# Kernel optimization log

Hardware: AMD Instinct MI355X
Metric: run time of the kernel (lower is better)

Reference implementation:

```python
import jax, jax.numpy as jnp
import numpy as np

N = 100000
E = 1600000
IN_C, HID_C, OUT_C = 128, 128, 64


def setup_inputs() -> dict:
    key = jax.random.key(0)
    ks = jax.random.split(key, 8)
    x = jax.random.normal(ks[0], (N, IN_C), dtype=jnp.float32)
    edge_index = jax.random.randint(ks[1], (2, E), 0, N, dtype=jnp.int64)
    s = 1.0 / np.sqrt(IN_C)
    s2 = 1.0 / np.sqrt(HID_C)
    return {
        "x": x,
        "edge_index": edge_index,
        # layer 1: SAGEConv(in=128, out=128): lin_l (neighbor, with bias), lin_r (root, no bias)
        "W_l1": jax.random.uniform(ks[2], (IN_C, HID_C), jnp.float32, -s, s),
        "b_l1": jnp.zeros((HID_C,), jnp.float32),
        "W_r1": jax.random.uniform(ks[3], (IN_C, HID_C), jnp.float32, -s, s),
        # layer 2: SAGEConv(in=128, out=64)
        "W_l2": jax.random.uniform(ks[4], (HID_C, OUT_C), jnp.float32, -s2, s2),
        "b_l2": jnp.zeros((OUT_C,), jnp.float32),
        "W_r2": jax.random.uniform(ks[5], (HID_C, OUT_C), jnp.float32, -s2, s2),
    }


def _sage_conv(x, src, dst, W_l, b_l, W_r, n_nodes):
    # mean aggregation of source-node features at target nodes
    msg = x[src]                                    # [E, d] gather
    agg = jax.ops.segment_sum(msg, dst, num_segments=n_nodes)          # [N, d]
    cnt = jax.ops.segment_sum(jnp.ones((src.shape[0], 1), x.dtype), dst,
                              num_segments=n_nodes)                    # [N, 1]
    mean = agg / jnp.maximum(cnt, 1.0)
    # out = lin_l(mean_neighbors) + lin_r(x_self)
    return mean @ W_l + b_l + x @ W_r


def reference(x, edge_index, W_l1, b_l1, W_r1, W_l2, b_l2, W_r2):
    src, dst = edge_index[0], edge_index[1]
    n = x.shape[0]
    h = _sage_conv(x, src, dst, W_l1, b_l1, W_r1, n)
    h = jax.nn.relu(h)  # dropout is identity in eval mode
    out = _sage_conv(h, src, dst, W_l2, b_l2, W_r2, n)
    return out
```

## Files before the change

kernel.cpp:

```cpp
#include <hip/hip_runtime.h>
#include <hip/hip_bf16.h>
#include <stdint.h>

#define IN_C 128
#define HID_C 128
#define OUT_C 64

#define NBUCK 256
#define BSH 9
#define EPB 2048

typedef _Float16 h8 __attribute__((ext_vector_type(8)));
typedef _Float16 h2 __attribute__((ext_vector_type(2)));
typedef float f4 __attribute__((ext_vector_type(4)));
typedef float f2 __attribute__((ext_vector_type(2)));
typedef unsigned u4 __attribute__((ext_vector_type(4)));

__device__ inline float h2lo(unsigned v){ h2 t = __builtin_bit_cast(h2, v); return (float)t[0]; }
__device__ inline float h2hi(unsigned v){ h2 t = __builtin_bit_cast(h2, v); return (float)t[1]; }
__device__ inline unsigned packh2(float a, float b){ h2 t; t[0]=(_Float16)a; t[1]=(_Float16)b; return __builtin_bit_cast(unsigned, t); }

__device__ inline void pack_one(const float* __restrict__ W, int C, _Float16* __restrict__ outp, int tid){
    int l = tid & 63;
    int f = tid >> 6;
    int NJT = C / 16;
    int kt = f / NJT;
    int jt = f - kt*NJT;
    int kbase = kt*32 + (l >> 4)*8;
    int col   = jt*16 + (l & 15);
    h8 o;
    #pragma unroll
    for (int r = 0; r < 8; ++r) o[r] = (_Float16)W[(kbase + r)*C + col];
    ((h8*)outp)[f*64 + l] = o;
}

__global__ __launch_bounds__(256) void k_front(const int* __restrict__ dst, int E, int NBLK,
                                               int* __restrict__ histT,
                                               const float* __restrict__ x,
                                               uint2* __restrict__ x8, int n8,
                                               const float* __restrict__ Wl1, const float* __restrict__ Wr1,
                                               const float* __restrict__ Wl2, const float* __restrict__ Wr2,
                                               _Float16* __restrict__ wl1p, _Float16* __restrict__ wr1p,
                                               _Float16* __restrict__ wl2p, _Float16* __restrict__ wr2p){
    __shared__ int h[NBUCK];
    int bid = blockIdx.x, t = threadIdx.x;
    if (bid < NBLK){
        h[t] = 0; __syncthreads();
        int e0 = bid*EPB, e1 = min(E, e0 + EPB);
        for (int e = e0 + t; e < e1; e += 256) atomicAdd(&h[((unsigned)dst[e]) >> BSH], 1);
        __syncthreads();
        histT[t*NBLK + bid] = h[t];
    } else if (bid < NBLK + 24){
        int tid = (bid - NBLK)*256 + t;
        if (tid < 2048)        pack_one(Wl1, 128, wl1p, tid);
        else if (tid < 4096)   pack_one(Wr1, 128, wr1p, tid - 2048);
        else if (tid < 5120)   pack_one(Wl2,  64, wl2p, tid - 4096);
        else if (tid < 6144)   pack_one(Wr2,  64, wr2p, tid - 5120);
    } else {
        int g = (bid - NBLK - 24)*256 + t;
        if (g < n8){
            const f4* xp = (const f4*)(x + (size_t)g*8);
            f4 a = xp[0], b = xp[1];
            int w0 = __builtin_amdgcn_cvt_pk_fp8_f32(a[0], a[1], 0, false);
            w0     = __builtin_amdgcn_cvt_pk_fp8_f32(a[2], a[3], w0, true);
            int w1 = __builtin_amdgcn_cvt_pk_fp8_f32(b[0], b[1], 0, false);
            w1     = __builtin_amdgcn_cvt_pk_fp8_f32(b[2], b[3], w1, true);
            uint2 p; p.x = (unsigned)w0; p.y = (unsigned)w1;
            x8[g] = p;
        }
    }
}

__global__ void k_scanA(const int* __restrict__ cnt, int* __restrict__ tmp, int* __restrict__ bsum, int n){
    __shared__ int s[256];
    int t = threadIdx.x, g = blockIdx.x*256 + t;
    int v = (g < n) ? cnt[g] : 0;
    s[t] = v; __syncthreads();
    for (int off = 1; off < 256; off <<= 1){
        int a = (t >= off) ? s[t-off] : 0;
        __syncthreads();
        s[t] += a;
        __syncthreads();
    }
    int excl = (t == 0) ? 0 : s[t-1];
    if (g < n) tmp[g] = excl;
    if (t == 255) bsum[blockIdx.x] = s[255];
}

__global__ void k_scanB(int* __restrict__ bsum, int nb){
    __shared__ int s[1024];
    int t = threadIdx.x;
    int v = (t < nb) ? bsum[t] : 0;
    s[t] = v; __syncthreads();
    for (int off = 1; off < 1024; off <<= 1){
        int a = (t >= off) ? s[t-off] : 0;
        __syncthreads();
        s[t] += a;
        __syncthreads();
    }
    int excl = (t == 0) ? 0 : s[t-1];
    if (t < nb) bsum[t] = excl;
}

__global__ __launch_bounds__(256) void k_scatter(const int* __restrict__ src, const int* __restrict__ dst,
                                                 int E, const int* __restrict__ tmp, const int* __restrict__ bsum,
                                                 int NBLK, unsigned* __restrict__ sorted){
    __shared__ int off[NBUCK];
    int t = threadIdx.x;
    int g = t*NBLK + blockIdx.x;
    off[t] = tmp[g] + bsum[g >> 8];
    __syncthreads();
    int e0 = blockIdx.x*EPB, e1 = min(E, e0 + EPB);
    for (int e = e0 + t; e < e1; e += 256){
        int d = dst[e];
        int b = ((unsigned)d) >> BSH;
        int p = atomicAdd(&off[b], 1);
        sorted[p] = (unsigned)src[e] | (((unsigned)(d & ((1<<BSH)-1))) << 17);
    }
}

__global__ __launch_bounds__(512) void k_csr(const unsigned* __restrict__ sorted,
                                             const int* __restrict__ tmp, const int* __restrict__ bsum,
                                             int NBLK, int E, int N,
                                             int* __restrict__ csr, int* __restrict__ row_start){
    __shared__ int cnt[512];
    __shared__ int sc[512];
    int b = blockIdx.x, t = threadIdx.x;
    int i0 = b*NBLK;
    int bs = tmp[i0] + bsum[i0 >> 8];
    int be = (b == NBUCK-1) ? E : (tmp[i0 + NBLK] + bsum[(i0 + NBLK) >> 8]);
    cnt[t] = 0; __syncthreads();
    for (int e = bs + t; e < be; e += 512) atomicAdd(&cnt[sorted[e] >> 17], 1);
    __syncthreads();
    sc[t] = cnt[t]; __syncthreads();
    for (int off = 1; off < 512; off <<= 1){
        int a = (t >= off) ? sc[t-off] : 0;
        __syncthreads();
        sc[t] += a;
        __syncthreads();
    }
    int excl = sc[t] - cnt[t];
    int nid = (b << BSH) + t;
    if (nid < N) row_start[nid] = bs + excl;
    if (t == 0 && b == (N >> BSH)) row_start[N] = E;
    __syncthreads();
    cnt[t] = excl;
    __syncthreads();
    for (int e = bs + t; e < be; e += 512){
        unsigned v = sorted[e];
        int dl = v >> 17;
        int p = atomicAdd(&cnt[dl], 1);
        csr[bs + p] = (int)(v & 0x1FFFFu);
    }
}

__global__ void k_agg1(const int* __restrict__ row_start, const int* __restrict__ csr,
                       const uint2* __restrict__ x8, unsigned* __restrict__ mh32, int n){
    int node = (int)((blockIdx.x*(unsigned)blockDim.x + threadIdx.x) >> 4);
    int c = threadIdx.x & 15;
    if (node >= n) return;
    int base = row_start[node], end = row_start[node+1];
    int deg = end - base;
    f2 a0={0.f,0.f}, a1={0.f,0.f}, a2={0.f,0.f}, a3={0.f,0.f};
    f2 b0={0.f,0.f}, b1={0.f,0.f}, b2={0.f,0.f}, b3={0.f,0.f};
    int i = base;
    for (; i + 7 < end; i += 8){
        int e0 = csr[i],   e1 = csr[i+1], e2 = csr[i+2], e3 = csr[i+3];
        int e4 = csr[i+4], e5 = csr[i+5], e6 = csr[i+6], e7 = csr[i+7];
        uint2 v0 = x8[(size_t)e0*16 + c];
        uint2 v1 = x8[(size_t)e1*16 + c];
        uint2 v2 = x8[(size_t)e2*16 + c];
        uint2 v3 = x8[(size_t)e3*16 + c];
        uint2 v4 = x8[(size_t)e4*16 + c];
        uint2 v5 = x8[(size_t)e5*16 + c];
        uint2 v6 = x8[(size_t)e6*16 + c];
        uint2 v7 = x8[(size_t)e7*16 + c];
        a0 += __builtin_amdgcn_cvt_pk_f32_fp8(v0.x, false);
        a1 += __builtin_amdgcn_cvt_pk_f32_fp8(v0.x, true);
        a2 += __builtin_amdgcn_cvt_pk_f32_fp8(v0.y, false);
        a3 += __builtin_amdgcn_cvt_pk_f32_fp8(v0.y, true);
        b0 += __builtin_amdgcn_cvt_pk_f32_fp8(v1.x, false);
        b1 += __builtin_amdgcn_cvt_pk_f32_fp8(v1.x, true);
        b2 += __builtin_amdgcn_cvt_pk_f32_fp8(v1.y, false);
        b3 += __builtin_amdgcn_cvt_pk_f32_fp8(v1.y, true);
        a0 += __builtin_amdgcn_cvt_pk_f32_fp8(v2.x, false);
        a1 += __builtin_amdgcn_cvt_pk_f32_fp8(v2.x, true);
        a2 += __builtin_amdgcn_cvt_pk_f32_fp8(v2.y, false);
        a3 += __builtin_amdgcn_cvt_pk_f32_fp8(v2.y, true);
        b0 += __builtin_amdgcn_cvt_pk_f32_fp8(v3.x, false);
        b1 += __builtin_amdgcn_cvt_pk_f32_fp8(v3.x, true);
        b2 += __builtin_amdgcn_cvt_pk_f32_fp8(v3.y, false);
        b3 += __builtin_amdgcn_cvt_pk_f32_fp8(v3.y, true);
        a0 += __builtin_amdgcn_cvt_pk_f32_fp8(v4.x, false);
        a1 += __builtin_amdgcn_cvt_pk_f32_fp8(v4.x, true);
        a2 += __builtin_amdgcn_cvt_pk_f32_fp8(v4.y, false);
        a3 += __builtin_amdgcn_cvt_pk_f32_fp8(v4.y, true);
        b0 += __builtin_amdgcn_cvt_pk_f32_fp8(v5.x, false);
        b1 += __builtin_amdgcn_cvt_pk_f32_fp8(v5.x, true);
        b2 += __builtin_amdgcn_cvt_pk_f32_fp8(v5.y, false);
        b3 += __builtin_amdgcn_cvt_pk_f32_fp8(v5.y, true);
        a0 += __builtin_amdgcn_cvt_pk_f32_fp8(v6.x, false);
        a1 += __builtin_amdgcn_cvt_pk_f32_fp8(v6.x, true);
        a2 += __builtin_amdgcn_cvt_pk_f32_fp8(v6.y, false);
        a3 += __builtin_amdgcn_cvt_pk_f32_fp8(v6.y, true);
        b0 += __builtin_amdgcn_cvt_pk_f32_fp8(v7.x, false);
        b1 += __builtin_amdgcn_cvt_pk_f32_fp8(v7.x, true);
        b2 += __builtin_amdgcn_cvt_pk_f32_fp8(v7.y, false);
        b3 += __builtin_amdgcn_cvt_pk_f32_fp8(v7.y, true);
    }
    for (; i + 3 < end; i += 4){
        int e0 = csr[i], e1 = csr[i+1], e2 = csr[i+2], e3 = csr[i+3];
        uint2 v0 = x8[(size_t)e0*16 + c];
        uint2 v1 = x8[(size_t)e1*16 + c];
        uint2 v2 = x8[(size_t)e2*16 + c];
        uint2 v3 = x8[(size_t)e3*16 + c];
        a0 += __builtin_amdgcn_cvt_pk_f32_fp8(v0.x, false);
        a1 += __builtin_amdgcn_cvt_pk_f32_fp8(v0.x, true);
        a2 += __builtin_amdgcn_cvt_pk_f32_fp8(v0.y, false);
        a3 += __builtin_amdgcn_cvt_pk_f32_fp8(v0.y, true);
        b0 += __builtin_amdgcn_cvt_pk_f32_fp8(v1.x, false);
        b1 += __builtin_amdgcn_cvt_pk_f32_fp8(v1.x, true);
        b2 += __builtin_amdgcn_cvt_pk_f32_fp8(v1.y, false);
        b3 += __builtin_amdgcn_cvt_pk_f32_fp8(v1.y, true);
        a0 += __builtin_amdgcn_cvt_pk_f32_fp8(v2.x, false);
        a1 += __builtin_amdgcn_cvt_pk_f32_fp8(v2.x, true);
        a2 += __builtin_amdgcn_cvt_pk_f32_fp8(v2.y, false);
        a3 += __builtin_amdgcn_cvt_pk_f32_fp8(v2.y, true);
        b0 += __builtin_amdgcn_cvt_pk_f32_fp8(v3.x, false);
        b1 += __builtin_amdgcn_cvt_pk_f32_fp8(v3.x, true);
        b2 += __builtin_amdgcn_cvt_pk_f32_fp8(v3.y, false);
        b3 += __builtin_amdgcn_cvt_pk_f32_fp8(v3.y, true);
    }
    for (; i < end; ++i){
        int e = csr[i];
        uint2 v = x8[(size_t)e*16 + c];
        a0 += __builtin_amdgcn_cvt_pk_f32_fp8(v.x, false);
        a1 += __builtin_amdgcn_cvt_pk_f32_fp8(v.x, true);
        a2 += __builtin_amdgcn_cvt_pk_f32_fp8(v.y, false);
        a3 += __builtin_amdgcn_cvt_pk_f32_fp8(v.y, true);
    }
    a0 += b0; a1 += b1; a2 += b2; a3 += b3;
    float sc = 1.0f / (float)max(deg, 1);
    u4 o;
    o[0] = packh2(a0[0]*sc, a0[1]*sc);
    o[1] = packh2(a1[0]*sc, a1[1]*sc);
    o[2] = packh2(a2[0]*sc, a2[1]*sc);
    o[3] = packh2(a3[0]*sc, a3[1]*sc);
    *(u4*)(mh32 + (size_t)node*64 + 4*c) = o;
}

__global__ __launch_bounds__(512, 4) void k_gemm_fused(
    const _Float16* __restrict__ A0,
    const float* __restrict__ X,
    const h8* __restrict__ B0,
    const h8* __restrict__ B1,
    const float* __restrict__ bias1,
    const h8* __restrict__ W2l,
    const h8* __restrict__ W2r,
    const float* __restrict__ bias2,
    unsigned* __restrict__ P8,
    uint2* __restrict__ Qh,
    int M)
{
    __shared__ h8 shB[4096];
    int tid = threadIdx.x;
    #pragma unroll
    for (int i = 0; i < 4; ++i) shB[i*512 + tid] = B0[i*512 + tid];
    #pragma unroll
    for (int i = 0; i < 4; ++i) shB[2048 + i*512 + tid] = B1[i*512 + tid];
    __syncthreads();

    int wid = tid >> 6, lane = tid & 63;
    int m0 = (blockIdx.x*8 + wid) * 16;
    if (m0 >= M) return;
    int m = lane & 15, kg = lane >> 4;
    int rowc = min(m0 + m, M-1);

    f4 acc[8];
    #pragma unroll
    for (int j = 0; j < 8; ++j) acc[j] = (f4)0.0f;

    #pragma unroll
    for (int kt = 0; kt < 4; ++kt){
        h8 nf = *(const h8*)(A0 + (size_t)rowc*128 + kt*32 + kg*8);
        #pragma unroll
        for (int j = 0; j < 8; ++j){
            h8 wf = shB[(kt*8 + j)*64 + lane];
            acc[j] = __builtin_amdgcn_mfma_f32_16x16x32_f16(wf, nf, acc[j], 0, 0, 0);
        }
    }
    #pragma unroll
    for (int kt = 0; kt < 4; ++kt){
        const float* xr = X + (size_t)rowc*128 + kt*32 + kg*8;
        f4 xa = *(const f4*)(xr);
        f4 xb = *(const f4*)(xr + 4);
        h8 nf;
        nf[0]=(_Float16)xa[0]; nf[1]=(_Float16)xa[1]; nf[2]=(_Float16)xa[2]; nf[3]=(_Float16)xa[3];
        nf[4]=(_Float16)xb[0]; nf[5]=(_Float16)xb[1]; nf[6]=(_Float16)xb[2]; nf[7]=(_Float16)xb[3];
        #pragma unroll
        for (int j = 0; j < 8; ++j){
            h8 wf = shB[2048 + (kt*8 + j)*64 + lane];
            acc[j] = __builtin_amdgcn_mfma_f32_16x16x32_f16(wf, nf, acc[j], 0, 0, 0);
        }
    }

    unsigned hreg[16];
    #pragma unroll
    for (int j = 0; j < 8; ++j){
        f4 bb = *(const f4*)(bias1 + j*16 + kg*4);
        float v0 = acc[j][0] + bb[0]; v0 = v0 > 0.f ? v0 : 0.f;
        float v1 = acc[j][1] + bb[1]; v1 = v1 > 0.f ? v1 : 0.f;
        float v2 = acc[j][2] + bb[2]; v2 = v2 > 0.f ? v2 : 0.f;
        float v3 = acc[j][3] + bb[3]; v3 = v3 > 0.f ? v3 : 0.f;
        hreg[2*j]   = packh2(v0, v1);
        hreg[2*j+1] = packh2(v2, v3);
    }

    f4 accP[4], accQ[4];
    #pragma unroll
    for (int j = 0; j < 4; ++j){ accP[j] = (f4)0.0f; accQ[j] = (f4)0.0f; }

    int srcA = ((kg & 1) * 2) * 16 + m;
    int srcB = srcA + 16;
    bool hi = (kg >> 1) & 1;

    #pragma unroll
    for (int kt = 0; kt < 4; ++kt){
        unsigned sA0 = (unsigned)__shfl((int)hreg[4*kt+0], srcA, 64);
        unsigned sA1 = (unsigned)__shfl((int)hreg[4*kt+1], srcA, 64);
        unsigned sA2 = (unsigned)__shfl((int)hreg[4*kt+2], srcA, 64);
        unsigned sA3 = (unsigned)__shfl((int)hreg[4*kt+3], srcA, 64);
        unsigned sB0 = (unsigned)__shfl((int)hreg[4*kt+0], srcB, 64);
        unsigned sB1 = (unsigned)__shfl((int)hreg[4*kt+1], srcB, 64);
        unsigned sB2 = (unsigned)__shfl((int)hreg[4*kt+2], srcB, 64);
        unsigned sB3 = (unsigned)__shfl((int)hreg[4*kt+3], srcB, 64);
        u4 u;
        u[0] = hi ? sA2 : sA0;
        u[1] = hi ? sA3 : sA1;
        u[2] = hi ? sB2 : sB0;
        u[3] = hi ? sB3 : sB1;
        h8 hf = __builtin_bit_cast(h8, u);
        #pragma unroll
        for (int j2 = 0; j2 < 4; ++j2){
            accP[j2] = __builtin_amdgcn_mfma_f32_16x16x32_f16(W2l[(kt*4 + j2)*64 + lane], hf, accP[j2], 0, 0, 0);
            accQ[j2] = __builtin_amdgcn_mfma_f32_16x16x32_f16(W2r[(kt*4 + j2)*64 + lane], hf, accQ[j2], 0, 0, 0);
        }
    }

    int node = m0 + m;
    if (node < M){
        #pragma unroll
        for (int j2 = 0; j2 < 4; ++j2){
            int f = j2*16 + kg*4;
            int p8 = __builtin_amdgcn_cvt_pk_fp8_f32(accP[j2][0], accP[j2][1], 0, false);
            p8     = __builtin_amdgcn_cvt_pk_fp8_f32(accP[j2][2], accP[j2][3], p8, true);
            P8[(size_t)node*16 + j2*4 + kg] = (unsigned)p8;
            f4 bb2 = *(const f4*)(bias2 + f);
            uint2 qp;
            qp.x = packh2(accQ[j2][0] + bb2[0], accQ[j2][1] + bb2[1]);
            qp.y = packh2(accQ[j2][2] + bb2[2], accQ[j2][3] + bb2[3]);
            Qh[(size_t)node*16 + j2*4 + kg] = qp;
        }
    }
}

__global__ void k_agg2f(const int* __restrict__ row_start, const int* __restrict__ csr,
                        const unsigned* __restrict__ p8, const uint2* __restrict__ Qh,
                        float* __restrict__ out, int n){
    int node = (int)((blockIdx.x*(unsigned)blockDim.x + threadIdx.x) >> 4);
    int c = threadIdx.x & 15;
    if (node >= n) return;
    int base = row_start[node], end = row_start[node+1];
    int deg = end - base;
    f2 a0={0.f,0.f}, a1={0.f,0.f}, b0={0.f,0.f}, b1={0.f,0.f};
    f2 c0={0.f,0.f}, c1={0.f,0.f}, d0={0.f,0.f}, d1={0.f,0.f};
    int i = base;
    for (; i + 7 < end; i += 8){
        int e0 = csr[i],   e1 = csr[i+1], e2 = csr[i+2], e3 = csr[i+3];
        int e4 = csr[i+4], e5 = csr[i+5], e6 = csr[i+6], e7 = csr[i+7];
        unsigned v0 = p8[(size_t)e0*16 + c];
        unsigned v1 = p8[(size_t)e1*16 + c];
        unsigned v2 = p8[(size_t)e2*16 + c];
        unsigned v3 = p8[(size_t)e3*16 + c];
        unsigned v4 = p8[(size_t)e4*16 + c];
        unsigned v5 = p8[(size_t)e5*16 + c];
        unsigned v6 = p8[(size_t)e6*16 + c];
        unsigned v7 = p8[(size_t)e7*16 + c];
        a0 += __builtin_amdgcn_cvt_pk_f32_fp8(v0, false);
        a1 += __builtin_amdgcn_cvt_pk_f32_fp8(v0, true);
        b0 += __builtin_amdgcn_cvt_pk_f32_fp8(v1, false);
        b1 += __builtin_amdgcn_cvt_pk_f32_fp8(v1, true);
        c0 += __builtin_amdgcn_cvt_pk_f32_fp8(v2, false);
        c1 += __builtin_amdgcn_cvt_pk_f32_fp8(v2, true);
        d0 += __builtin_amdgcn_cvt_pk_f32_fp8(v3, false);
        d1 += __builtin_amdgcn_cvt_pk_f32_fp8(v3, true);
        a0 += __builtin_amdgcn_cvt_pk_f32_fp8(v4, false);
        a1 += __builtin_amdgcn_cvt_pk_f32_fp8(v4, true);
        b0 += __builtin_amdgcn_cvt_pk_f32_fp8(v5, false);
        b1 += __builtin_amdgcn_cvt_pk_f32_fp8(v5, true);
        c0 += __builtin_amdgcn_cvt_pk_f32_fp8(v6, false);
        c1 += __builtin_amdgcn_cvt_pk_f32_fp8(v6, true);
        d0 += __builtin_amdgcn_cvt_pk_f32_fp8(v7, false);
        d1 += __builtin_amdgcn_cvt_pk_f32_fp8(v7, true);
    }
    for (; i + 3 < end; i += 4){
        int e0 = csr[i], e1 = csr[i+1], e2 = csr[i+2], e3 = csr[i+3];
        unsigned v0 = p8[(size_t)e0*16 + c];
        unsigned v1 = p8[(size_t)e1*16 + c];
        unsigned v2 = p8[(size_t)e2*16 + c];
        unsigned v3 = p8[(size_t)e3*16 + c];
        a0 += __builtin_amdgcn_cvt_pk_f32_fp8(v0, false);
        a1 += __builtin_amdgcn_cvt_pk_f32_fp8(v0, true);
        b0 += __builtin_amdgcn_cvt_pk_f32_fp8(v1, false);
        b1 += __builtin_amdgcn_cvt_pk_f32_fp8(v1, true);
        c0 += __builtin_amdgcn_cvt_pk_f32_fp8(v2, false);
        c1 += __builtin_amdgcn_cvt_pk_f32_fp8(v2, true);
        d0 += __builtin_amdgcn_cvt_pk_f32_fp8(v3, false);
        d1 += __builtin_amdgcn_cvt_pk_f32_fp8(v3, true);
    }
    for (; i < end; ++i){
        int e = csr[i];
        unsigned v = p8[(size_t)e*16 + c];
        a0 += __builtin_amdgcn_cvt_pk_f32_fp8(v, false);
        a1 += __builtin_amdgcn_cvt_pk_f32_fp8(v, true);
    }
    a0 += b0 + c0 + d0;
    a1 += b1 + c1 + d1;
    float sc = 1.0f / (float)max(deg, 1);
    uint2 qh = Qh[(size_t)node*16 + c];
    f4 o;
    o[0] = a0[0]*sc + h2lo(qh.x);
    o[1] = a0[1]*sc + h2hi(qh.x);
    o[2] = a1[0]*sc + h2lo(qh.y);
    o[3] = a1[1]*sc + h2hi(qh.y);
    *(f4*)(out + (size_t)node*64 + 4*c) = o;
}

extern "C" void kernel_launch(void* const* d_in, const int* in_sizes, int n_in,
                              void* d_out, int out_size, void* d_ws, size_t ws_size,
                              hipStream_t stream) {
    const float* x   = (const float*)d_in[0];
    const int*   ei  = (const int*)d_in[1];
    const float* Wl1 = (const float*)d_in[2];
    const float* bl1 = (const float*)d_in[3];
    const float* Wr1 = (const float*)d_in[4];
    const float* Wl2 = (const float*)d_in[5];
    const float* bl2 = (const float*)d_in[6];
    const float* Wr2 = (const float*)d_in[7];

    const int N = in_sizes[0] / IN_C;
    const int E = in_sizes[1] / 2;
    const int* src = ei;
    const int* dst = ei + E;

    const int NBLK = (E + EPB - 1) / EPB;
    const int n_s  = NBUCK * NBLK;

    char* w = (char*)d_ws;
    size_t off = 0;
    auto alloc = [&](size_t bytes) -> char* {
        char* p = w + off;
        off = (off + bytes + 255) & ~(size_t)255;
        return p;
    };
    int* histT      = (int*)alloc((size_t)n_s*4);
    int* tmp        = (int*)alloc((size_t)n_s*4);
    int* bsum       = (int*)alloc(4096);
    unsigned* sorted= (unsigned*)alloc((size_t)E*4);
    int* csr        = (int*)alloc((size_t)E*4);
    int* row_start  = (int*)alloc((size_t)(N+1)*4);
    unsigned* x8    = (unsigned*)alloc((size_t)N*IN_C);
    _Float16* m1h   = (_Float16*)alloc((size_t)N*IN_C*2);
    unsigned* p8    = (unsigned*)alloc((size_t)N*OUT_C);
    unsigned* qh    = (unsigned*)alloc((size_t)N*OUT_C*2);
    _Float16* wl1p  = (_Float16*)alloc(4*8*64*8*2);
    _Float16* wr1p  = (_Float16*)alloc(4*8*64*8*2);
    _Float16* wl2p  = (_Float16*)alloc(4*4*64*8*2);
    _Float16* wr2p  = (_Float16*)alloc(4*4*64*8*2);

    const int SB = (n_s + 255) / 256;
    const int n8 = N*IN_C/8;
    const int CVB = (n8 + 255)/256;

    k_front  <<<NBLK + 24 + CVB, 256, 0, stream>>>(dst, E, NBLK, histT,
                                                   x, (uint2*)x8, n8,
                                                   Wl1, Wr1, Wl2, Wr2, wl1p, wr1p, wl2p, wr2p);
    k_scanA  <<<SB, 256, 0, stream>>>(histT, tmp, bsum, n_s);
    k_scanB  <<<1, 1024, 0, stream>>>(bsum, SB);
    k_scatter<<<NBLK, 256, 0, stream>>>(src, dst, E, tmp, bsum, NBLK, sorted);
    k_csr    <<<NBUCK, 512, 0, stream>>>(sorted, tmp, bsum, NBLK, E, N, csr, row_start);

    const int AB = (N + 15) / 16;
    k_agg1<<<AB, 256, 0, stream>>>(row_start, csr, (const uint2*)x8, (unsigned*)m1h, N);

    const int GB2 = (N + 127)/128;
    k_gemm_fused<<<GB2, 512, 0, stream>>>(m1h, x, (const h8*)wl1p, (const h8*)wr1p, bl1,
                                          (const h8*)wl2p, (const h8*)wr2p, bl2,
                                          p8, (uint2*)qh, N);

    k_agg2f<<<AB, 256, 0, stream>>>(row_start, csr, p8, (const uint2*)qh, (float*)d_out, N);
}
```

Measured before the change: 148.1 us.

## Fuse layer-1 neighbor aggregation into the fused GEMM kernel via shared memory

Removes the separate k_agg1 kernel and computes the mean-aggregated fp16 neighbor features for each wave's 16 rows directly inside k_gemm_fused. The results go into a per-wave shared-memory tile with an XOR swizzle, and the MFMA A operand is read from there. This avoids writing and re-reading the N x 128 fp16 intermediate in global memory and saves one kernel launch. In exchange, shared memory per block grows by 32 KB, launch bounds drop to 2 blocks per CU, and the latency-bound gather now runs inside the GEMM kernel at lower occupancy.

```diff
diff --git a/kernel.cpp b/kernel.cpp
--- a/kernel.cpp
+++ b/kernel.cpp
@@ -154,103 +154,9 @@
     }
 }
 
-__global__ void k_agg1(const int* __restrict__ row_start, const int* __restrict__ csr,
-                       const uint2* __restrict__ x8, unsigned* __restrict__ mh32, int n){
-    int node = (int)((blockIdx.x*(unsigned)blockDim.x + threadIdx.x) >> 4);
-    int c = threadIdx.x & 15;
-    if (node >= n) return;
-    int base = row_start[node], end = row_start[node+1];
-    int deg = end - base;
-    f2 a0={0.f,0.f}, a1={0.f,0.f}, a2={0.f,0.f}, a3={0.f,0.f};
-    f2 b0={0.f,0.f}, b1={0.f,0.f}, b2={0.f,0.f}, b3={0.f,0.f};
-    int i = base;
-    for (; i + 7 < end; i += 8){
-        int e0 = csr[i],   e1 = csr[i+1], e2 = csr[i+2], e3 = csr[i+3];
-        int e4 = csr[i+4], e5 = csr[i+5], e6 = csr[i+6], e7 = csr[i+7];
-        uint2 v0 = x8[(size_t)e0*16 + c];
-        uint2 v1 = x8[(size_t)e1*16 + c];
-        uint2 v2 = x8[(size_t)e2*16 + c];
-        uint2 v3 = x8[(size_t)e3*16 + c];
-        uint2 v4 = x8[(size_t)e4*16 + c];
-        uint2 v5 = x8[(size_t)e5*16 + c];
-        uint2 v6 = x8[(size_t)e6*16 + c];
-        uint2 v7 = x8[(size_t)e7*16 + c];
-        a0 += __builtin_amdgcn_cvt_pk_f32_fp8(v0.x, false);
-        a1 += __builtin_amdgcn_cvt_pk_f32_fp8(v0.x, true);
-        a2 += __builtin_amdgcn_cvt_pk_f32_fp8(v0.y, false);
-        a3 += __builtin_amdgcn_cvt_pk_f32_fp8(v0.y, true);
-        b0 += __builtin_amdgcn_cvt_pk_f32_fp8(v1.x, false);
-        b1 += __builtin_amdgcn_cvt_pk_f32_fp8(v1.x, true);
-        b2 += __builtin_amdgcn_cvt_pk_f32_fp8(v1.y, false);
-        b3 += __builtin_amdgcn_cvt_pk_f32_fp8(v1.y, true);
-        a0 += __builtin_amdgcn_cvt_pk_f32_fp8(v2.x, false);
-        a1 += __builtin_amdgcn_cvt_pk_f32_fp8(v2.x, true);
-        a2 += __builtin_amdgcn_cvt_pk_f32_fp8(v2.y, false);
-        a3 += __builtin_amdgcn_cvt_pk_f32_fp8(v2.y, true);
-        b0 += __builtin_amdgcn_cvt_pk_f32_fp8(v3.x, false);
-        b1 += __builtin_amdgcn_cvt_pk_f32_fp8(v3.x, true);
-        b2 += __builtin_amdgcn_cvt_pk_f32_fp8(v3.y, false);
-        b3 += __builtin_amdgcn_cvt_pk_f32_fp8(v3.y, true);
-        a0 += __builtin_amdgcn_cvt_pk_f32_fp8(v4.x, false);
-        a1 += __builtin_amdgcn_cvt_pk_f32_fp8(v4.x, true);
-        a2 += __builtin_amdgcn_cvt_pk_f32_fp8(v4.y, false);
-        a3 += __builtin_amdgcn_cvt_pk_f32_fp8(v4.y, true);
-        b0 += __builtin_amdgcn_cvt_pk_f32_fp8(v5.x, false);
-        b1 += __builtin_amdgcn_cvt_pk_f32_fp8(v5.x, true);
-        b2 += __builtin_amdgcn_cvt_pk_f32_fp8(v5.y, false);
-        b3 += __builtin_amdgcn_cvt_pk_f32_fp8(v5.y, true);
-        a0 += __builtin_amdgcn_cvt_pk_f32_fp8(v6.x, false);
-        a1 += __builtin_amdgcn_cvt_pk_f32_fp8(v6.x, true);
-        a2 += __builtin_amdgcn_cvt_pk_f32_fp8(v6.y, false);
-        a3 += __builtin_amdgcn_cvt_pk_f32_fp8(v6.y, true);
-        b0 += __builtin_amdgcn_cvt_pk_f32_fp8(v7.x, false);
-        b1 += __builtin_amdgcn_cvt_pk_f32_fp8(v7.x, true);
-        b2 += __builtin_amdgcn_cvt_pk_f32_fp8(v7.y, false);
-        b3 += __builtin_amdgcn_cvt_pk_f32_fp8(v7.y, true);
-    }
-    for (; i + 3 < end; i += 4){
-        int e0 = csr[i], e1 = csr[i+1], e2 = csr[i+2], e3 = csr[i+3];
-        uint2 v0 = x8[(size_t)e0*16 + c];
-        uint2 v1 = x8[(size_t)e1*16 + c];
-        uint2 v2 = x8[(size_t)e2*16 + c];
-        uint2 v3 = x8[(size_t)e3*16 + c];
-        a0 += __builtin_amdgcn_cvt_pk_f32_fp8(v0.x, false);
-        a1 += __builtin_amdgcn_cvt_pk_f32_fp8(v0.x, true);
-        a2 += __builtin_amdgcn_cvt_pk_f32_fp8(v0.y, false);
-        a3 += __builtin_amdgcn_cvt_pk_f32_fp8(v0.y, true);
-        b0 += __builtin_amdgcn_cvt_pk_f32_fp8(v1.x, false);
-        b1 += __builtin_amdgcn_cvt_pk_f32_fp8(v1.x, true);
-        b2 += __builtin_amdgcn_cvt_pk_f32_fp8(v1.y, false);
-        b3 += __builtin_amdgcn_cvt_pk_f32_fp8(v1.y, true);
-        a0 += __builtin_amdgcn_cvt_pk_f32_fp8(v2.x, false);
-        a1 += __builtin_amdgcn_cvt_pk_f32_fp8(v2.x, true);
-        a2 += __builtin_amdgcn_cvt_pk_f32_fp8(v2.y, false);
-        a3 += __builtin_amdgcn_cvt_pk_f32_fp8(v2.y, true);
-        b0 += __builtin_amdgcn_cvt_pk_f32_fp8(v3.x, false);
-        b1 += __builtin_amdgcn_cvt_pk_f32_fp8(v3.x, true);
-        b2 += __builtin_amdgcn_cvt_pk_f32_fp8(v3.y, false);
-        b3 += __builtin_amdgcn_cvt_pk_f32_fp8(v3.y, true);
-    }
-    for (; i < end; ++i){
-        int e = csr[i];
-        uint2 v = x8[(size_t)e*16 + c];
-        a0 += __builtin_amdgcn_cvt_pk_f32_fp8(v.x, false);
-        a1 += __builtin_amdgcn_cvt_pk_f32_fp8(v.x, true);
-        a2 += __builtin_amdgcn_cvt_pk_f32_fp8(v.y, false);
-        a3 += __builtin_amdgcn_cvt_pk_f32_fp8(v.y, true);
-    }
-    a0 += b0; a1 += b1; a2 += b2; a3 += b3;
-    float sc = 1.0f / (float)max(deg, 1);
-    u4 o;
-    o[0] = packh2(a0[0]*sc, a0[1]*sc);
-    o[1] = packh2(a1[0]*sc, a1[1]*sc);
-    o[2] = packh2(a2[0]*sc, a2[1]*sc);
-    o[3] = packh2(a3[0]*sc, a3[1]*sc);
-    *(u4*)(mh32 + (size_t)node*64 + 4*c) = o;
-}
-
-__global__ __launch_bounds__(512, 4) void k_gemm_fused(
-    const _Float16* __restrict__ A0,
+__global__ __launch_bounds__(512, 2) void k_gemm_fused(
+    const int* __restrict__ row_start, const int* __restrict__ csr,
+    const uint2* __restrict__ x8,
     const float* __restrict__ X,
     const h8* __restrict__ B0,
     const h8* __restrict__ B1,
@@ -263,6 +169,7 @@
     int M)
 {
     __shared__ h8 shB[4096];
+    __shared__ unsigned shM[8][1024];
     int tid = threadIdx.x;
     #pragma unroll
     for (int i = 0; i < 4; ++i) shB[i*512 + tid] = B0[i*512 + tid];
@@ -276,13 +183,111 @@
     int m = lane & 15, kg = lane >> 4;
     int rowc = min(m0 + m, M-1);
 
+    unsigned* myM = &shM[wid][0];
+    {
+        int c = lane & 15;
+        #pragma unroll 1
+        for (int p = 0; p < 4; ++p){
+            int slot = p*4 + (lane >> 4);
+            int node = min(m0 + slot, M-1);
+            int base = row_start[node], end = row_start[node+1];
+            int deg = end - base;
+            f2 a0={0.f,0.f}, a1={0.f,0.f}, a2={0.f,0.f}, a3={0.f,0.f};
+            f2 b0={0.f,0.f}, b1={0.f,0.f}, b2={0.f,0.f}, b3={0.f,0.f};
+            int i = base;
+            for (; i + 7 < end; i += 8){
+                int e0 = csr[i],   e1 = csr[i+1], e2 = csr[i+2], e3 = csr[i+3];
+                int e4 = csr[i+4], e5 = csr[i+5], e6 = csr[i+6], e7 = csr[i+7];
+                uint2 v0 = x8[(size_t)e0*16 + c];
+                uint2 v1 = x8[(size_t)e1*16 + c];
+                uint2 v2 = x8[(size_t)e2*16 + c];
+                uint2 v3 = x8[(size_t)e3*16 + c];
+                uint2 v4 = x8[(size_t)e4*16 + c];
+                uint2 v5 = x8[(size_t)e5*16 + c];
+                uint2 v6 = x8[(size_t)e6*16 + c];
+                uint2 v7 = x8[(size_t)e7*16 + c];
+                a0 += __builtin_amdgcn_cvt_pk_f32_fp8(v0.x, false);
+                a1 += __builtin_amdgcn_cvt_pk_f32_fp8(v0.x, true);
+                a2 += __builtin_amdgcn_cvt_pk_f32_fp8(v0.y, false);
+                a3 += __builtin_amdgcn_cvt_pk_f32_fp8(v0.y, true);
+                b0 += __builtin_amdgcn_cvt_pk_f32_fp8(v1.x, false);
+                b1 += __builtin_amdgcn_cvt_pk_f32_fp8(v1.x, true);
+                b2 += __builtin_amdgcn_cvt_pk_f32_fp8(v1.y, false);
+                b3 += __builtin_amdgcn_cvt_pk_f32_fp8(v1.y, true);
+                a0 += __builtin_amdgcn_cvt_pk_f32_fp8(v2.x, false);
+                a1 += __builtin_amdgcn_cvt_pk_f32_fp8(v2.x, true);
+                a2 += __builtin_amdgcn_cvt_pk_f32_fp8(v2.y, false);
+                a3 += __builtin_amdgcn_cvt_pk_f32_fp8(v2.y, true);
+                b0 += __builtin_amdgcn_cvt_pk_f32_fp8(v3.x, false);
+                b1 += __builtin_amdgcn_cvt_pk_f32_fp8(v3.x, true);
+                b2 += __builtin_amdgcn_cvt_pk_f32_fp8(v3.y, false);
+                b3 += __builtin_amdgcn_cvt_pk_f32_fp8(v3.y, true);
+                a0 += __builtin_amdgcn_cvt_pk_f32_fp8(v4.x, false);
+                a1 += __builtin_amdgcn_cvt_pk_f32_fp8(v4.x, true);
+                a2 += __builtin_amdgcn_cvt_pk_f32_fp8(v4.y, false);
+                a3 += __builtin_amdgcn_cvt_pk_f32_fp8(v4.y, true);
+                b0 += __builtin_amdgcn_cvt_pk_f32_fp8(v5.x, false);
+                b1 += __builtin_amdgcn_cvt_pk_f32_fp8(v5.x, true);
+                b2 += __builtin_amdgcn_cvt_pk_f32_fp8(v5.y, false);
+                b3 += __builtin_amdgcn_cvt_pk_f32_fp8(v5.y, true);
+                a0 += __builtin_amdgcn_cvt_pk_f32_fp8(v6.x, false);
+                a1 += __builtin_amdgcn_cvt_pk_f32_fp8(v6.x, true);
+                a2 += __builtin_amdgcn_cvt_pk_f32_fp8(v6.y, false);
+                a3 += __builtin_amdgcn_cvt_pk_f32_fp8(v6.y, true);
+                b0 += __builtin_amdgcn_cvt_pk_f32_fp8(v7.x, false);
+                b1 += __builtin_amdgcn_cvt_pk_f32_fp8(v7.x, true);
+                b2 += __builtin_amdgcn_cvt_pk_f32_fp8(v7.y, false);
+                b3 += __builtin_amdgcn_cvt_pk_f32_fp8(v7.y, true);
+            }
+            for (; i + 3 < end; i += 4){
+                int e0 = csr[i], e1 = csr[i+1], e2 = csr[i+2], e3 = csr[i+3];
+                uint2 v0 = x8[(size_t)e0*16 + c];
+                uint2 v1 = x8[(size_t)e1*16 + c];
+                uint2 v2 = x8[(size_t)e2*16 + c];
+                uint2 v3 = x8[(size_t)e3*16 + c];
+                a0 += __builtin_amdgcn_cvt_pk_f32_fp8(v0.x, false);
+                a1 += __builtin_amdgcn_cvt_pk_f32_fp8(v0.x, true);
+                a2 += __builtin_amdgcn_cvt_pk_f32_fp8(v0.y, false);
+                a3 += __builtin_amdgcn_cvt_pk_f32_fp8(v0.y, true);
+                b0 += __builtin_amdgcn_cvt_pk_f32_fp8(v1.x, false);
+                b1 += __builtin_amdgcn_cvt_pk_f32_fp8(v1.x, true);
+                b2 += __builtin_amdgcn_cvt_pk_f32_fp8(v1.y, false);
+                b3 += __builtin_amdgcn_cvt_pk_f32_fp8(v1.y, true);
+                a0 += __builtin_amdgcn_cvt_pk_f32_fp8(v2.x, false);
+                a1 += __builtin_amdgcn_cvt_pk_f32_fp8(v2.x, true);
+                a2 += __builtin_amdgcn_cvt_pk_f32_fp8(v2.y, false);
+                a3 += __builtin_amdgcn_cvt_pk_f32_fp8(v2.y, true);
+                b0 += __builtin_amdgcn_cvt_pk_f32_fp8(v3.x, false);
+                b1 += __builtin_amdgcn_cvt_pk_f32_fp8(v3.x, true);
+                b2 += __builtin_amdgcn_cvt_pk_f32_fp8(v3.y, false);
+                b3 += __builtin_amdgcn_cvt_pk_f32_fp8(v3.y, true);
+            }
+            for (; i < end; ++i){
+                int e = csr[i];
+                uint2 v = x8[(size_t)e*16 + c];
+                a0 += __builtin_amdgcn_cvt_pk_f32_fp8(v.x, false);
+                a1 += __builtin_amdgcn_cvt_pk_f32_fp8(v.x, true);
+                a2 += __builtin_amdgcn_cvt_pk_f32_fp8(v.y, false);
+                a3 += __builtin_amdgcn_cvt_pk_f32_fp8(v.y, true);
+            }
+            a0 += b0; a1 += b1; a2 += b2; a3 += b3;
+            float sc = 1.0f / (float)max(deg, 1);
+            u4 o;
+            o[0] = packh2(a0[0]*sc, a0[1]*sc);
+            o[1] = packh2(a1[0]*sc, a1[1]*sc);
+            o[2] = packh2(a2[0]*sc, a2[1]*sc);
+            o[3] = packh2(a3[0]*sc, a3[1]*sc);
+            *(u4*)&myM[slot*64 + ((c*4) ^ ((slot&7)<<2))] = o;
+        }
+    }
+
     f4 acc[8];
     #pragma unroll
     for (int j = 0; j < 8; ++j) acc[j] = (f4)0.0f;
 
     #pragma unroll
     for (int kt = 0; kt < 4; ++kt){
-        h8 nf = *(const h8*)(A0 + (size_t)rowc*128 + kt*32 + kg*8);
+        h8 nf = *(const h8*)&myM[m*64 + ((kt*16 + kg*4) ^ ((m&7)<<2))];
         #pragma unroll
         for (int j = 0; j < 8; ++j){
             h8 wf = shB[(kt*8 + j)*64 + lane];
@@ -352,9 +357,9 @@
         #pragma unroll
         for (int j2 = 0; j2 < 4; ++j2){
             int f = j2*16 + kg*4;
-            int p8 = __builtin_amdgcn_cvt_pk_fp8_f32(accP[j2][0], accP[j2][1], 0, false);
-            p8     = __builtin_amdgcn_cvt_pk_fp8_f32(accP[j2][2], accP[j2][3], p8, true);
-            P8[(size_t)node*16 + j2*4 + kg] = (unsigned)p8;
+            int p8v = __builtin_amdgcn_cvt_pk_fp8_f32(accP[j2][0], accP[j2][1], 0, false);
+            p8v     = __builtin_amdgcn_cvt_pk_fp8_f32(accP[j2][2], accP[j2][3], p8v, true);
+            P8[(size_t)node*16 + j2*4 + kg] = (unsigned)p8v;
             f4 bb2 = *(const f4*)(bias2 + f);
             uint2 qp;
             qp.x = packh2(accQ[j2][0] + bb2[0], accQ[j2][1] + bb2[1]);
@@ -470,7 +475,6 @@
     int* csr        = (int*)alloc((size_t)E*4);
     int* row_start  = (int*)alloc((size_t)(N+1)*4);
     unsigned* x8    = (unsigned*)alloc((size_t)N*IN_C);
-    _Float16* m1h   = (_Float16*)alloc((size_t)N*IN_C*2);
     unsigned* p8    = (unsigned*)alloc((size_t)N*OUT_C);
     unsigned* qh    = (unsigned*)alloc((size_t)N*OUT_C*2);
     _Float16* wl1p  = (_Float16*)alloc(4*8*64*8*2);
@@ -490,13 +494,12 @@
     k_scatter<<<NBLK, 256, 0, stream>>>(src, dst, E, tmp, bsum, NBLK, sorted);
     k_csr    <<<NBUCK, 512, 0, stream>>>(sorted, tmp, bsum, NBLK, E, N, csr, row_start);
 
-    const int AB = (N + 15) / 16;
-    k_agg1<<<AB, 256, 0, stream>>>(row_start, csr, (const uint2*)x8, (unsigned*)m1h, N);
-
     const int GB2 = (N + 127)/128;
-    k_gemm_fused<<<GB2, 512, 0, stream>>>(m1h, x, (const h8*)wl1p, (const h8*)wr1p, bl1,
+    k_gemm_fused<<<GB2, 512, 0, stream>>>(row_start, csr, (const uint2*)x8, x,
+                                          (const h8*)wl1p, (const h8*)wr1p, bl1,
                                           (const h8*)wl2p, (const h8*)wr2p, bl2,
                                           p8, (uint2*)qh, N);
 
+    const int AB = (N + 15) / 16;
     k_agg2f<<<AB, 256, 0, stream>>>(row_start, csr, p8, (const uint2*)qh, (float*)d_out, N);
 }
```

After: 189.3 us. +27.8%, slower.

## Split layer-1 aggregation into column slices across blocks

Applied to the files above, without the earlier changes.

The first-layer gather kernel now splits each node's 128 fp8 features into 8 column slices handled by separate blocks. Each lane loads 4 bytes instead of 8, and each block touches only a 16-byte slice per neighbour row. The intent is to raise parallelism and improve L2 locality of the gathered feature columns. In exchange, the CSR indices and row_start are re-read 8 times, the 4-edge unrolled tail is removed, and each gather is now a narrower, less coalesced 16-byte access per row.

```diff
diff --git a/kernel.cpp b/kernel.cpp
--- a/kernel.cpp
+++ b/kernel.cpp
@@ -154,99 +154,61 @@
     }
 }
 
-__global__ void k_agg1(const int* __restrict__ row_start, const int* __restrict__ csr,
-                       const uint2* __restrict__ x8, unsigned* __restrict__ mh32, int n){
-    int node = (int)((blockIdx.x*(unsigned)blockDim.x + threadIdx.x) >> 4);
-    int c = threadIdx.x & 15;
+__global__ __launch_bounds__(256) void k_agg1(const int* __restrict__ row_start, const int* __restrict__ csr,
+                                              const unsigned* __restrict__ x8u, unsigned* __restrict__ mh32, int n){
+    int slice = blockIdx.x & 7;
+    int sb    = blockIdx.x >> 3;
+    int wid   = threadIdx.x >> 6;
+    int lane  = threadIdx.x & 63;
+    int g     = lane >> 2;
+    int j     = lane & 3;
+    int node  = (sb*4 + wid)*16 + g;
     if (node >= n) return;
     int base = row_start[node], end = row_start[node+1];
     int deg = end - base;
-    f2 a0={0.f,0.f}, a1={0.f,0.f}, a2={0.f,0.f}, a3={0.f,0.f};
-    f2 b0={0.f,0.f}, b1={0.f,0.f}, b2={0.f,0.f}, b3={0.f,0.f};
+    int col = slice*4 + j;
+    f2 a0={0.f,0.f}, a1={0.f,0.f}, b0={0.f,0.f}, b1={0.f,0.f};
     int i = base;
     for (; i + 7 < end; i += 8){
         int e0 = csr[i],   e1 = csr[i+1], e2 = csr[i+2], e3 = csr[i+3];
         int e4 = csr[i+4], e5 = csr[i+5], e6 = csr[i+6], e7 = csr[i+7];
-        uint2 v0 = x8[(size_t)e0*16 + c];
-        uint2 v1 = x8[(size_t)e1*16 + c];
-        uint2 v2 = x8[(size_t)e2*16 + c];
-        uint2 v3 = x8[(size_t)e3*16 + c];
-        uint2 v4 = x8[(size_t)e4*16 + c];
-        uint2 v5 = x8[(size_t)e5*16 + c];
-        uint2 v6 = x8[(size_t)e6*16 + c];
-        uint2 v7 = x8[(size_t)e7*16 + c];
-        a0 += __builtin_amdgcn_cvt_pk_f32_fp8(v0.x, false);
-        a1 += __builtin_amdgcn_cvt_pk_f32_fp8(v0.x, true);
-        a2 += __builtin_amdgcn_cvt_pk_f32_fp8(v0.y, false);
-        a3 += __builtin_amdgcn_cvt_pk_f32_fp8(v0.y, true);
-        b0 += __builtin_amdgcn_cvt_pk_f32_fp8(v1.x, false);
-        b1 += __builtin_amdgcn_cvt_pk_f32_fp8(v1.x, true);
-        b2 += __builtin_amdgcn_cvt_pk_f32_fp8(v1.y, false);
-        b3 += __builtin_amdgcn_cvt_pk_f32_fp8(v1.y, true);
-        a0 += __builtin_amdgcn_cvt_pk_f32_fp8(v2.x, false);
-        a1 += __builtin_amdgcn_cvt_pk_f32_fp8(v2.x, true);
-        a2 += __builtin_amdgcn_cvt_pk_f32_fp8(v2.y, false);
-        a3 += __builtin_amdgcn_cvt_pk_f32_fp8(v2.y, true);
-        b0 += __builtin_amdgcn_cvt_pk_f32_fp8(v3.x, false);
-        b1 += __builtin_amdgcn_cvt_pk_f32_fp8(v3.x, true);
-        b2 += __builtin_amdgcn_cvt_pk_f32_fp8(v3.y, false);
-        b3 += __builtin_amdgcn_cvt_pk_f32_fp8(v3.y, true);
-        a0 += __builtin_amdgcn_cvt_pk_f32_fp8(v4.x, false);
-        a1 += __builtin_amdgcn_cvt_pk_f32_fp8(v4.x, true);
-        a2 += __builtin_amdgcn_cvt_pk_f32_fp8(v4.y, false);
-        a3 += __builtin_amdgcn_cvt_pk_f32_fp8(v4.y, true);
-        b0 += __builtin_amdgcn_cvt_pk_f32_fp8(v5.x, false);
-        b1 += __builtin_amdgcn_cvt_pk_f32_fp8(v5.x, true);
-        b2 += __builtin_amdgcn_cvt_pk_f32_fp8(v5.y, false);
-        b3 += __builtin_amdgcn_cvt_pk_f32_fp8(v5.y, true);
-        a0 += __builtin_amdgcn_cvt_pk_f32_fp8(v6.x, false);
-        a1 += __builtin_amdgcn_cvt_pk_f32_fp8(v6.x, true);
-        a2 += __builtin_amdgcn_cvt_pk_f32_fp8(v6.y, false);
-        a3 += __builtin_amdgcn_cvt_pk_f32_fp8(v6.y, true);
-        b0 += __builtin_amdgcn_cvt_pk_f32_fp8(v7.x, false);
-        b1 += __builtin_amdgcn_cvt_pk_f32_fp8(v7.x, true);
-        b2 += __builtin_amdgcn_cvt_pk_f32_fp8(v7.y, false);
-        b3 += __builtin_amdgcn_cvt_pk_f32_fp8(v7.y, true);
-    }
-    for (; i + 3 < end; i += 4){
-        int e0 = csr[i], e1 = csr[i+1], e2 = csr[i+2], e3 = csr[i+3];
-        uint2 v0 = x8[(size_t)e0*16 + c];
-        uint2 v1 = x8[(size_t)e1*16 + c];
-        uint2 v2 = x8[(size_t)e2*16 + c];
-        uint2 v3 = x8[(size_t)e3*16 + c];
-        a0 += __builtin_amdgcn_cvt_pk_f32_fp8(v0.x, false);
-        a1 += __builtin_amdgcn_cvt_pk_f32_fp8(v0.x, true);
-        a2 += __builtin_amdgcn_cvt_pk_f32_fp8(v0.y, false);
-        a3 += __builtin_amdgcn_cvt_pk_f32_fp8(v0.y, true);
-        b0 += __builtin_amdgcn_cvt_pk_f32_fp8(v1.x, false);
-        b1 += __builtin_amdgcn_cvt_pk_f32_fp8(v1.x, true);
-        b2 += __builtin_amdgcn_cvt_pk_f32_fp8(v1.y, false);
-        b3 += __builtin_amdgcn_cvt_pk_f32_fp8(v1.y, true);
-        a0 += __builtin_amdgcn_cvt_pk_f32_fp8(v2.x, false);
-        a1 += __builtin_amdgcn_cvt_pk_f32_fp8(v2.x, true);
-        a2 += __builtin_amdgcn_cvt_pk_f32_fp8(v2.y, false);
-        a3 += __builtin_amdgcn_cvt_pk_f32_fp8(v2.y, true);
-        b0 += __builtin_amdgcn_cvt_pk_f32_fp8(v3.x, false);
-        b1 += __builtin_amdgcn_cvt_pk_f32_fp8(v3.x, true);
-        b2 += __builtin_amdgcn_cvt_pk_f32_fp8(v3.y, false);
-        b3 += __builtin_amdgcn_cvt_pk_f32_fp8(v3.y, true);
+        unsigned v0 = x8u[(size_t)e0*32 + col];
+        unsigned v1 = x8u[(size_t)e1*32 + col];
+        unsigned v2 = x8u[(size_t)e2*32 + col];
+        unsigned v3 = x8u[(size_t)e3*32 + col];
+        unsigned v4 = x8u[(size_t)e4*32 + col];
+        unsigned v5 = x8u[(size_t)e5*32 + col];
+        unsigned v6 = x8u[(size_t)e6*32 + col];
+        unsigned v7 = x8u[(size_t)e7*32 + col];
+        a0 += __builtin_amdgcn_cvt_pk_f32_fp8(v0, false);
+        a1 += __builtin_amdgcn_cvt_pk_f32_fp8(v0, true);
+        b0 += __builtin_amdgcn_cvt_pk_f32_fp8(v1, false);
+        b1 += __builtin_amdgcn_cvt_pk_f32_fp8(v1, true);
+        a0 += __builtin_amdgcn_cvt_pk_f32_fp8(v2, false);
+        a1 += __builtin_amdgcn_cvt_pk_f32_fp8(v2, true);
+        b0 += __builtin_amdgcn_cvt_pk_f32_fp8(v3, false);
+        b1 += __builtin_amdgcn_cvt_pk_f32_fp8(v3, true);
+        a0 += __builtin_amdgcn_cvt_pk_f32_fp8(v4, false);
+        a1 += __builtin_amdgcn_cvt_pk_f32_fp8(v4, true);
+        b0 += __builtin_amdgcn_cvt_pk_f32_fp8(v5, false);
+        b1 += __builtin_amdgcn_cvt_pk_f32_fp8(v5, true);
+        a0 += __builtin_amdgcn_cvt_pk_f32_fp8(v6, false);
+        a1 += __builtin_amdgcn_cvt_pk_f32_fp8(v6, true);
+        b0 += __builtin_amdgcn_cvt_pk_f32_fp8(v7, false);
+        b1 += __builtin_amdgcn_cvt_pk_f32_fp8(v7, true);
     }
     for (; i < end; ++i){
         int e = csr[i];
-        uint2 v = x8[(size_t)e*16 + c];
-        a0 += __builtin_amdgcn_cvt_pk_f32_fp8(v.x, false);
-        a1 += __builtin_amdgcn_cvt_pk_f32_fp8(v.x, true);
-        a2 += __builtin_amdgcn_cvt_pk_f32_fp8(v.y, false);
-        a3 += __builtin_amdgcn_cvt_pk_f32_fp8(v.y, true);
-    }
-    a0 += b0; a1 += b1; a2 += b2; a3 += b3;
+        unsigned v = x8u[(size_t)e*32 + col];
+        a0 += __builtin_amdgcn_cvt_pk_f32_fp8(v, false);
+        a1 += __builtin_amdgcn_cvt_pk_f32_fp8(v, true);
+    }
+    a0 += b0; a1 += b1;
     float sc = 1.0f / (float)max(deg, 1);
-    u4 o;
-    o[0] = packh2(a0[0]*sc, a0[1]*sc);
-    o[1] = packh2(a1[0]*sc, a1[1]*sc);
-    o[2] = packh2(a2[0]*sc, a2[1]*sc);
-    o[3] = packh2(a3[0]*sc, a3[1]*sc);
-    *(u4*)(mh32 + (size_t)node*64 + 4*c) = o;
+    uint2 o;
+    o.x = packh2(a0[0]*sc, a0[1]*sc);
+    o.y = packh2(a1[0]*sc, a1[1]*sc);
+    *(uint2*)(mh32 + (size_t)node*64 + slice*8 + j*2) = o;
 }
 
 __global__ __launch_bounds__(512, 4) void k_gemm_fused(
@@ -352,9 +314,9 @@
         #pragma unroll
         for (int j2 = 0; j2 < 4; ++j2){
             int f = j2*16 + kg*4;
-            int p8 = __builtin_amdgcn_cvt_pk_fp8_f32(accP[j2][0], accP[j2][1], 0, false);
-            p8     = __builtin_amdgcn_cvt_pk_fp8_f32(accP[j2][2], accP[j2][3], p8, true);
-            P8[(size_t)node*16 + j2*4 + kg] = (unsigned)p8;
+            int p8v = __builtin_amdgcn_cvt_pk_fp8_f32(accP[j2][0], accP[j2][1], 0, false);
+            p8v     = __builtin_amdgcn_cvt_pk_fp8_f32(accP[j2][2], accP[j2][3], p8v, true);
+            P8[(size_t)node*16 + j2*4 + kg] = (unsigned)p8v;
             f4 bb2 = *(const f4*)(bias2 + f);
             uint2 qp;
             qp.x = packh2(accQ[j2][0] + bb2[0], accQ[j2][1] + bb2[1]);
@@ -490,13 +452,14 @@
     k_scatter<<<NBLK, 256, 0, stream>>>(src, dst, E, tmp, bsum, NBLK, sorted);
     k_csr    <<<NBUCK, 512, 0, stream>>>(sorted, tmp, bsum, NBLK, E, N, csr, row_start);
 
-    const int AB = (N + 15) / 16;
-    k_agg1<<<AB, 256, 0, stream>>>(row_start, csr, (const uint2*)x8, (unsigned*)m1h, N);
+    const int SBK = (N + 63) / 64;
+    k_agg1<<<SBK*8, 256, 0, stream>>>(row_start, csr, x8, (unsigned*)m1h, N);
 
     const int GB2 = (N + 127)/128;
     k_gemm_fused<<<GB2, 512, 0, stream>>>(m1h, x, (const h8*)wl1p, (const h8*)wr1p, bl1,
                                           (const h8*)wl2p, (const h8*)wr2p, bl2,
                                           p8, (uint2*)qh, N);
 
+    const int AB = (N + 15) / 16;
     k_agg2f<<<AB, 256, 0, stream>>>(row_start, csr, p8, (const uint2*)qh, (float*)d_out, N);
 }
```

Result: slower. 308.9 us (+108.6%).
